# Kernel optimization log

Hardware: AMD Instinct MI355X
Metric: run time of the kernel (lower is better)

Reference implementation:

```python
import jax, jax.numpy as jnp
import numpy as np

EMBED_DIM = 4096
POLY_PTS = 32
POLY_DIM = POLY_PTS * 2  # 64
LN_EPS = 1e-5


def setup_inputs() -> dict:
    key = jax.random.key(0)
    ks = jax.random.split(key, 12)
    B, N, Dmax = 8, 1024, POLY_DIM
    s = 0.02
    return {
        "prompts": jax.random.normal(ks[0], (B, N, Dmax), dtype=jnp.float32),
        "prompt_types": jax.random.randint(ks[1], (B, N), 0, 3, dtype=jnp.int64),
        # point encoder: Linear(2, E)
        "point_w": jax.random.normal(ks[2], (EMBED_DIM, 2), dtype=jnp.float32) * s,
        "point_b": jax.random.normal(ks[3], (EMBED_DIM,), dtype=jnp.float32) * s,
        # box encoder: Linear(4, E)
        "box_w": jax.random.normal(ks[4], (EMBED_DIM, 4), dtype=jnp.float32) * s,
        "box_b": jax.random.normal(ks[5], (EMBED_DIM,), dtype=jnp.float32) * s,
        # polygon encoder: Linear(64,E) -> LayerNorm(E) -> ReLU -> Linear(E,E)
        "poly_w1": jax.random.normal(ks[6], (EMBED_DIM, POLY_DIM), dtype=jnp.float32) * s,
        "poly_b1": jax.random.normal(ks[7], (EMBED_DIM,), dtype=jnp.float32) * s,
        "ln_gamma": jnp.ones((EMBED_DIM,), dtype=jnp.float32),
        "ln_beta": jnp.zeros((EMBED_DIM,), dtype=jnp.float32),
        "poly_w2": jax.random.normal(ks[8], (EMBED_DIM, EMBED_DIM), dtype=jnp.float32) * s,
        "poly_b2": jax.random.normal(ks[9], (EMBED_DIM,), dtype=jnp.float32) * s,
        # type embedding table (3, E)
        "type_emb": jax.random.normal(ks[10], (3, EMBED_DIM), dtype=jnp.float32) * s,
    }


def _layernorm(x, gamma, beta):
    mu = jnp.mean(x, axis=-1, keepdims=True)
    var = jnp.mean(jnp.square(x - mu), axis=-1, keepdims=True)
    return (x - mu) * jax.lax.rsqrt(var + LN_EPS) * gamma + beta


def reference(prompts, prompt_types, point_w, point_b, box_w, box_b,
              poly_w1, poly_b1, ln_gamma, ln_beta, poly_w2, poly_b2, type_emb):
    # Per-type expert encodings computed densely, then selected by type mask
    # (same math as torch's masked gather -> linear -> scatter).
    pt = jnp.einsum('bnd,ed->bne', prompts[..., :2], point_w) + point_b + type_emb[0]
    bx = jnp.einsum('bnd,ed->bne', prompts[..., :4], box_w) + box_b + type_emb[1]
    h = jnp.einsum('bnd,ed->bne', prompts[..., :POLY_DIM], poly_w1) + poly_b1
    h = jax.nn.relu(_layernorm(h, ln_gamma, ln_beta))
    pg = jnp.einsum('bnd,ed->bne', h, poly_w2) + poly_b2 + type_emb[2]
    t = prompt_types[..., None]
    zeros = jnp.zeros_like(pt)
    out = jnp.where(t == 0, pt, zeros) + jnp.where(t == 1, bx, zeros) + jnp.where(t == 2, pg, zeros)
    return out
```

## Files before the change

kernel.cpp:

```cpp
#include <hip/hip_runtime.h>

#define EMBED 4096
#define NTOK 8192
#define LN_EPS 1e-5f

typedef float f4_t __attribute__((ext_vector_type(4)));
typedef __bf16 bf16x8 __attribute__((ext_vector_type(8)));
typedef unsigned short us8_t __attribute__((ext_vector_type(8)));

__device__ __forceinline__ unsigned short f2bf(float f) {
    unsigned int u = __float_as_uint(f);
    u += 0x7fffu + ((u >> 16) & 1u);
    return (unsigned short)(u >> 16);
}

typedef const __attribute__((address_space(1))) unsigned int gas_t;
typedef __attribute__((address_space(3))) unsigned int las_t;

__device__ __forceinline__ void gl_lds16(const void* g, void* l) {
    __builtin_amdgcn_global_load_lds((gas_t*)g, (las_t*)l, 16, 0, 0);
}

__global__ void k_compact(const int* __restrict__ types, int* __restrict__ idx,
                          int* __restrict__ counters) {
    __shared__ int cnt;
    if (threadIdx.x == 0) cnt = 0;
    __syncthreads();
    for (int i = threadIdx.x; i < NTOK; i += 1024) {
        if (types[i] == 2) {
            int s = atomicAdd(&cnt, 1);
            idx[s] = i;
        }
    }
    __syncthreads();
    if (threadIdx.x == 0) {
        counters[0] = cnt;
        counters[1] = (cnt + 127) & ~127;
    }
}

__global__ __launch_bounds__(256) void k_prepG(const float* __restrict__ w1,
                                               const float* __restrict__ b1,
                                               float* __restrict__ G,
                                               float* __restrict__ cbar) {
    int i = blockIdx.x;
    int t = threadIdx.x;
    float part[65];
#pragma unroll
    for (int j = 0; j < 65; ++j) part[j] = 0.f;
    for (int e = t; e < EMBED; e += 256) {
        const f4_t* row4 = (const f4_t*)(w1 + (size_t)e * 64);
        float be = b1[e];
        float ai = (i < 64) ? w1[(size_t)e * 64 + i] : ((i == 64) ? be : 1.f);
#pragma unroll
        for (int q = 0; q < 16; ++q) {
            f4_t r = row4[q];
            part[4 * q + 0] += ai * r.x;
            part[4 * q + 1] += ai * r.y;
            part[4 * q + 2] += ai * r.z;
            part[4 * q + 3] += ai * r.w;
        }
        part[64] += ai * be;
    }
#pragma unroll
    for (int j = 0; j < 65; ++j) {
        float v = part[j];
        v += __shfl_down(v, 32);
        v += __shfl_down(v, 16);
        v += __shfl_down(v, 8);
        v += __shfl_down(v, 4);
        v += __shfl_down(v, 2);
        v += __shfl_down(v, 1);
        part[j] = v;
    }
    __shared__ float sw[4][66];
    int wave = t >> 6, lane = t & 63;
    if (lane == 0) {
#pragma unroll
        for (int j = 0; j < 65; ++j) sw[wave][j] = part[j];
    }
    __syncthreads();
    if (t < 65) {
        float s = (sw[0][t] + sw[1][t] + sw[2][t] + sw[3][t]) * (1.f / 4096.f);
        if (i < 65) G[i * 65 + t] = s;
        else        cbar[t] = s;
    }
}

__global__ __launch_bounds__(256) void k_conv(const float* __restrict__ src,
                                              unsigned short* __restrict__ dst) {
    int i = blockIdx.x * 256 + threadIdx.x;
    const f4_t* in4 = (const f4_t*)src;
    f4_t v0 = in4[(size_t)i * 2];
    f4_t v1 = in4[(size_t)i * 2 + 1];
    us8_t o;
    o[0] = f2bf(v0.x); o[1] = f2bf(v0.y); o[2] = f2bf(v0.z); o[3] = f2bf(v0.w);
    o[4] = f2bf(v1.x); o[5] = f2bf(v1.y); o[6] = f2bf(v1.z); o[7] = f2bf(v1.w);
    *(us8_t*)(dst + (size_t)i * 8) = o;
}

__global__ __launch_bounds__(256) void k_enc01(const float* __restrict__ prompts,
                                               const int* __restrict__ types,
                                               const float* __restrict__ pw,
                                               const float* __restrict__ pb,
                                               const float* __restrict__ bw,
                                               const float* __restrict__ bb,
                                               const float* __restrict__ temb,
                                               float* __restrict__ out) {
    int token = blockIdx.x;
    int ty = types[token];
    if (ty >= 2) return;
    const float* x = prompts + (size_t)token * 64;
    float x0 = x[0], x1 = x[1], x2 = x[2], x3 = x[3];
    f4_t* o4 = (f4_t*)(out + (size_t)token * EMBED);
    int t = threadIdx.x;
    if (ty == 0) {
        const f4_t* w4 = (const f4_t*)pw;
        const f4_t* b4 = (const f4_t*)pb;
        const f4_t* te4 = (const f4_t*)temb;
#pragma unroll
        for (int j = 0; j < 4; ++j) {
            int e4 = t + 256 * j;
            f4_t wa = w4[e4 * 2], wb = w4[e4 * 2 + 1];
            f4_t bv = b4[e4], tv = te4[e4];
            f4_t r;
            r.x = x0 * wa.x + x1 * wa.y + bv.x + tv.x;
            r.y = x0 * wa.z + x1 * wa.w + bv.y + tv.y;
            r.z = x0 * wb.x + x1 * wb.y + bv.z + tv.z;
            r.w = x0 * wb.z + x1 * wb.w + bv.w + tv.w;
            o4[e4] = r;
        }
    } else {
        const f4_t* w4 = (const f4_t*)bw;
        const f4_t* b4 = (const f4_t*)bb;
        const f4_t* te4 = (const f4_t*)(temb + EMBED);
#pragma unroll
        for (int j = 0; j < 4; ++j) {
            int e4 = t + 256 * j;
            f4_t w0 = w4[e4 * 4 + 0], w1v = w4[e4 * 4 + 1];
            f4_t w2v = w4[e4 * 4 + 2], w3v = w4[e4 * 4 + 3];
            f4_t bv = b4[e4], tv = te4[e4];
            f4_t r;
            r.x = x0 * w0.x + x1 * w0.y + x2 * w0.z + x3 * w0.w + bv.x + tv.x;
            r.y = x0 * w1v.x + x1 * w1v.y + x2 * w1v.z + x3 * w1v.w + bv.y + tv.y;
            r.z = x0 * w2v.x + x1 * w2v.y + x2 * w2v.z + x3 * w2v.w + bv.z + tv.z;
            r.w = x0 * w3v.x + x1 * w3v.y + x2 * w3v.z + x3 * w3v.w + bv.w + tv.w;
            o4[e4] = r;
        }
    }
}

__global__ __launch_bounds__(256) void k_stats(const float* __restrict__ prompts,
                                               const int* __restrict__ idx,
                                               const int* __restrict__ counters,
                                               const float* __restrict__ cbar,
                                               const float* __restrict__ G,
                                               float* __restrict__ mu,
                                               float* __restrict__ rstd,
                                               unsigned short* __restrict__ xbuf) {
    int count = counters[0], padded = counters[1];
    int base = blockIdx.x * 4;
    if (base >= padded) return;
    __shared__ float sG[65 * 65];
    __shared__ __align__(16) float xs[4][66];
    int t = threadIdx.x;
    for (int v = t; v < 65 * 65; v += 256) sG[v] = G[v];
    int r = t >> 6, lane = t & 63;
    int m = base + r;
    bool vld = (m < count);
    float xv = vld ? prompts[(size_t)idx[m] * 64 + lane] : 0.f;
    xs[r][lane] = xv;
    if (lane == 0) xs[r][64] = vld ? 1.f : 0.f;
    xbuf[(size_t)m * 64 + lane] = vld ? f2bf(xv) : (unsigned short)0;
    __syncthreads();
    float mu_p, m2_p;
    {
        float xi = xs[r][lane];
        mu_p = cbar[lane] * xi;
        const float* Gr = sG + lane * 65;
        float rd = 0.f;
        for (int j = 0; j < 65; ++j) rd += Gr[j] * xs[r][j];
        m2_p = xi * rd;
    }
    if (lane == 0) {
        float xi = xs[r][64];
        mu_p += cbar[64] * xi;
        const float* Gr = sG + 64 * 65;
        float rd = 0.f;
        for (int j = 0; j < 65; ++j) rd += Gr[j] * xs[r][j];
        m2_p += xi * rd;
    }
    for (int off = 32; off > 0; off >>= 1) {
        mu_p += __shfl_down(mu_p, off);
        m2_p += __shfl_down(m2_p, off);
    }
    if (lane == 0) {
        if (vld) {
            mu[m] = mu_p;
            rstd[m] = rsqrtf(fmaxf(m2_p - mu_p * mu_p, 0.f) + LN_EPS);
        } else {
            mu[m] = 0.f;
            rstd[m] = 0.f;
        }
    }
}

__global__ __launch_bounds__(256) void k_lin1m(const unsigned short* __restrict__ xbuf,
                                               const unsigned short* __restrict__ w1b,
                                               const int* __restrict__ counters,
                                               const float* __restrict__ b1,
                                               const float* __restrict__ gamma,
                                               const float* __restrict__ beta,
                                               const float* __restrict__ mu,
                                               const float* __restrict__ rstd,
                                               unsigned short* __restrict__ hbuf) {
    int padded = counters[1];
    int m0 = blockIdx.y * 128;
    if (m0 >= padded) return;
    int n0 = blockIdx.x * 128;

    __shared__ unsigned short At[128 * 32];
    __shared__ unsigned short Bt[128 * 32];

    int t = threadIdx.x;
    int lane = t & 63, wave = t >> 6;
    int wm = (wave >> 1) * 64;
    int wn = (wave & 1) * 64;

    int srow = t >> 2, skg = t & 3;
    const unsigned short* Ag = xbuf + (size_t)(m0 + srow) * 64 + skg * 8;
    const unsigned short* Bg = w1b + (size_t)(n0 + srow) * 64 + skg * 8;
    char* AtC = (char*)At;
    char* BtC = (char*)Bt;
    int ldsw = (t & ~63) * 16;

    f4_t acc[4][4];
#pragma unroll
    for (int i = 0; i < 4; ++i)
#pragma unroll
        for (int j = 0; j < 4; ++j) acc[i][j] = (f4_t)0.f;

    int fr = lane & 15;
    int quad = lane >> 4;

#pragma unroll
    for (int k0 = 0; k0 < 64; k0 += 32) {
        __syncthreads();
        gl_lds16(Ag + k0,            AtC + ldsw);
        gl_lds16(Ag + 64 * 64 + k0,  AtC + 4096 + ldsw);
        gl_lds16(Bg + k0,            BtC + ldsw);
        gl_lds16(Bg + 64 * 64 + k0,  BtC + 4096 + ldsw);
        __syncthreads();

        bf16x8 a[4], b[4];
#pragma unroll
        for (int i = 0; i < 4; ++i) {
            a[i] = *(const bf16x8*)(AtC + (wm + i * 16 + fr) * 64 + quad * 16);
            b[i] = *(const bf16x8*)(BtC + (wn + i * 16 + fr) * 64 + quad * 16);
        }
#pragma unroll
        for (int i = 0; i < 4; ++i)
#pragma unroll
            for (int j = 0; j < 4; ++j)
                acc[i][j] = __builtin_amdgcn_mfma_f32_16x16x32_bf16(a[i], b[j], acc[i][j], 0, 0, 0);
    }

#pragma unroll
    for (int i = 0; i < 4; ++i) {
#pragma unroll
        for (int r = 0; r < 4; ++r) {
            int grow = m0 + wm + i * 16 + quad * 4 + r;
            float muv = mu[grow], rsv = rstd[grow];
            unsigned short* hrow = hbuf + (size_t)grow * EMBED;
#pragma unroll
            for (int j = 0; j < 4; ++j) {
                int gcol = n0 + wn + j * 16 + fr;
                float h = (acc[i][j][r] + b1[gcol] - muv) * rsv * gamma[gcol] + beta[gcol];
                hrow[gcol] = f2bf(fmaxf(h, 0.f));
            }
        }
    }
}

__global__ __launch_bounds__(256) void k_gemm(const unsigned short* __restrict__ hbuf,
                                              const unsigned short* __restrict__ w2b,
                                              const int* __restrict__ idx,
                                              const int* __restrict__ counters,
                                              const float* __restrict__ b2,
                                              const float* __restrict__ te2,
                                              float* __restrict__ out) {
    int count = counters[0], padded = counters[1];
    int m0 = blockIdx.y * 128;
    if (m0 >= padded) return;
    int n0 = blockIdx.x * 128;

    __shared__ unsigned short At[128 * 32];
    __shared__ unsigned short Bt[128 * 32];

    int t = threadIdx.x;
    int lane = t & 63, wave = t >> 6;
    int wm = (wave >> 1) * 64;
    int wn = (wave & 1) * 64;

    int srow = t >> 2, skg = t & 3;
    const unsigned short* Ag = hbuf + (size_t)(m0 + srow) * EMBED + skg * 8;
    const unsigned short* Bg = w2b + (size_t)(n0 + srow) * EMBED + skg * 8;
    char* AtC = (char*)At;
    char* BtC = (char*)Bt;
    int ldsw = (t & ~63) * 16;

    f4_t acc[4][4];
#pragma unroll
    for (int i = 0; i < 4; ++i)
#pragma unroll
        for (int j = 0; j < 4; ++j) acc[i][j] = (f4_t)0.f;

    int fr = lane & 15;
    int quad = lane >> 4;

    for (int k0 = 0; k0 < EMBED; k0 += 32) {
        __syncthreads();
        gl_lds16(Ag + k0,               AtC + ldsw);
        gl_lds16(Ag + 64 * EMBED + k0,  AtC + 4096 + ldsw);
        gl_lds16(Bg + k0,               BtC + ldsw);
        gl_lds16(Bg + 64 * EMBED + k0,  BtC + 4096 + ldsw);
        __syncthreads();

        bf16x8 a[4], b[4];
#pragma unroll
        for (int i = 0; i < 4; ++i) {
            a[i] = *(const bf16x8*)(AtC + (wm + i * 16 + fr) * 64 + quad * 16);
            b[i] = *(const bf16x8*)(BtC + (wn + i * 16 + fr) * 64 + quad * 16);
        }
#pragma unroll
        for (int i = 0; i < 4; ++i)
#pragma unroll
            for (int j = 0; j < 4; ++j)
                acc[i][j] = __builtin_amdgcn_mfma_f32_16x16x32_bf16(a[i], b[j], acc[i][j], 0, 0, 0);
    }

#pragma unroll
    for (int i = 0; i < 4; ++i) {
#pragma unroll
        for (int r = 0; r < 4; ++r) {
            int grow = m0 + wm + i * 16 + quad * 4 + r;
            if (grow < count) {
                float* orow = out + (size_t)idx[grow] * EMBED;
#pragma unroll
                for (int j = 0; j < 4; ++j) {
                    int gcol = n0 + wn + j * 16 + fr;
                    orow[gcol] = acc[i][j][r] + b2[gcol] + te2[gcol];
                }
            }
        }
    }
}

extern "C" void kernel_launch(void* const* d_in, const int* in_sizes, int n_in,
                              void* d_out, int out_size, void* d_ws, size_t ws_size,
                              hipStream_t stream) {
    const float* prompts  = (const float*)d_in[0];
    const int*   types    = (const int*)d_in[1];
    const float* point_w  = (const float*)d_in[2];
    const float* point_b  = (const float*)d_in[3];
    const float* box_w    = (const float*)d_in[4];
    const float* box_b    = (const float*)d_in[5];
    const float* poly_w1  = (const float*)d_in[6];
    const float* poly_b1  = (const float*)d_in[7];
    const float* ln_g     = (const float*)d_in[8];
    const float* ln_b     = (const float*)d_in[9];
    const float* poly_w2  = (const float*)d_in[10];
    const float* poly_b2  = (const float*)d_in[11];
    const float* type_emb = (const float*)d_in[12];
    float* out = (float*)d_out;

    char* ws = (char*)d_ws;
    int*   counters = (int*)ws;
    int*   idx      = (int*)(ws + 256);
    float* cbar     = (float*)(ws + 33280);
    float* G        = (float*)(ws + 33792);
    float* muarr    = (float*)(ws + 51200);
    float* rstdarr  = (float*)(ws + 84224);
    unsigned short* xbuf = (unsigned short*)(ws + 131072);
    unsigned short* w1b  = (unsigned short*)(ws + 131072 + 1048576);
    unsigned short* w2b  = (unsigned short*)(ws + 2097152);
    unsigned short* hbuf = (unsigned short*)(ws + 2097152 + (size_t)EMBED * EMBED * 2);

    k_compact<<<1, 1024, 0, stream>>>(types, idx, counters);
    k_prepG<<<66, 256, 0, stream>>>(poly_w1, poly_b1, G, cbar);
    k_conv<<<EMBED * EMBED / (256 * 8), 256, 0, stream>>>(poly_w2, w2b);
    k_conv<<<EMBED * 64 / (256 * 8), 256, 0, stream>>>(poly_w1, w1b);
    k_enc01<<<NTOK, 256, 0, stream>>>(prompts, types, point_w, point_b,
                                      box_w, box_b, type_emb, out);
    k_stats<<<NTOK / 4, 256, 0, stream>>>(prompts, idx, counters, cbar, G,
                                          muarr, rstdarr, xbuf);
    k_lin1m<<<dim3(EMBED / 128, NTOK / 128), 256, 0, stream>>>(
        xbuf, w1b, counters, poly_b1, ln_g, ln_b, muarr, rstdarr, hbuf);
    k_gemm<<<dim3(EMBED / 128, NTOK / 128), 256, 0, stream>>>(
        hbuf, w2b, idx, counters, poly_b2, type_emb + 2 * EMBED, out);
}
```

Measured before the change: 388.4 us.

## Fuse prep kernels into one launch and stage 64-wide K tiles in GEMMs

Merges the compaction, G/cbar precompute, both bf16 weight conversions and the point/box encoder into one block-indexed prep kernel. This removes four launches and lets the independent pieces run concurrently. The G precompute now splits its 65 output columns across waves, cutting per-thread register arrays from 65 to 17 entries. Both GEMMs now load two 32-wide K slices per barrier pair, halving the synchronisations in the main 4096-K loop, at the cost of double the LDS per block.

```diff
diff --git a/kernel.cpp b/kernel.cpp
--- a/kernel.cpp
+++ b/kernel.cpp
@@ -3,6 +3,9 @@
 #define EMBED 4096
 #define NTOK 8192
 #define LN_EPS 1e-5f
+
+#define NB_CONVW2 (EMBED * EMBED / (256 * 8))
+#define NB_CONVW1 (EMBED * 64 / (256 * 8))
 
 typedef float f4_t __attribute__((ext_vector_type(4)));
 typedef __bf16 bf16x8 __attribute__((ext_vector_type(8)));
@@ -21,75 +24,9 @@
     __builtin_amdgcn_global_load_lds((gas_t*)g, (las_t*)l, 16, 0, 0);
 }
 
-__global__ void k_compact(const int* __restrict__ types, int* __restrict__ idx,
-                          int* __restrict__ counters) {
-    __shared__ int cnt;
-    if (threadIdx.x == 0) cnt = 0;
-    __syncthreads();
-    for (int i = threadIdx.x; i < NTOK; i += 1024) {
-        if (types[i] == 2) {
-            int s = atomicAdd(&cnt, 1);
-            idx[s] = i;
-        }
-    }
-    __syncthreads();
-    if (threadIdx.x == 0) {
-        counters[0] = cnt;
-        counters[1] = (cnt + 127) & ~127;
-    }
-}
-
-__global__ __launch_bounds__(256) void k_prepG(const float* __restrict__ w1,
-                                               const float* __restrict__ b1,
-                                               float* __restrict__ G,
-                                               float* __restrict__ cbar) {
-    int i = blockIdx.x;
-    int t = threadIdx.x;
-    float part[65];
-#pragma unroll
-    for (int j = 0; j < 65; ++j) part[j] = 0.f;
-    for (int e = t; e < EMBED; e += 256) {
-        const f4_t* row4 = (const f4_t*)(w1 + (size_t)e * 64);
-        float be = b1[e];
-        float ai = (i < 64) ? w1[(size_t)e * 64 + i] : ((i == 64) ? be : 1.f);
-#pragma unroll
-        for (int q = 0; q < 16; ++q) {
-            f4_t r = row4[q];
-            part[4 * q + 0] += ai * r.x;
-            part[4 * q + 1] += ai * r.y;
-            part[4 * q + 2] += ai * r.z;
-            part[4 * q + 3] += ai * r.w;
-        }
-        part[64] += ai * be;
-    }
-#pragma unroll
-    for (int j = 0; j < 65; ++j) {
-        float v = part[j];
-        v += __shfl_down(v, 32);
-        v += __shfl_down(v, 16);
-        v += __shfl_down(v, 8);
-        v += __shfl_down(v, 4);
-        v += __shfl_down(v, 2);
-        v += __shfl_down(v, 1);
-        part[j] = v;
-    }
-    __shared__ float sw[4][66];
-    int wave = t >> 6, lane = t & 63;
-    if (lane == 0) {
-#pragma unroll
-        for (int j = 0; j < 65; ++j) sw[wave][j] = part[j];
-    }
-    __syncthreads();
-    if (t < 65) {
-        float s = (sw[0][t] + sw[1][t] + sw[2][t] + sw[3][t]) * (1.f / 4096.f);
-        if (i < 65) G[i * 65 + t] = s;
-        else        cbar[t] = s;
-    }
-}
-
-__global__ __launch_bounds__(256) void k_conv(const float* __restrict__ src,
-                                              unsigned short* __restrict__ dst) {
-    int i = blockIdx.x * 256 + threadIdx.x;
+__device__ __forceinline__ void conv_body(const float* __restrict__ src,
+                                          unsigned short* __restrict__ dst,
+                                          int i) {
     const f4_t* in4 = (const f4_t*)src;
     f4_t v0 = in4[(size_t)i * 2];
     f4_t v1 = in4[(size_t)i * 2 + 1];
@@ -99,53 +36,136 @@
     *(us8_t*)(dst + (size_t)i * 8) = o;
 }
 
-__global__ __launch_bounds__(256) void k_enc01(const float* __restrict__ prompts,
-                                               const int* __restrict__ types,
-                                               const float* __restrict__ pw,
-                                               const float* __restrict__ pb,
-                                               const float* __restrict__ bw,
-                                               const float* __restrict__ bb,
-                                               const float* __restrict__ temb,
-                                               float* __restrict__ out) {
-    int token = blockIdx.x;
-    int ty = types[token];
-    if (ty >= 2) return;
-    const float* x = prompts + (size_t)token * 64;
-    float x0 = x[0], x1 = x[1], x2 = x[2], x3 = x[3];
-    f4_t* o4 = (f4_t*)(out + (size_t)token * EMBED);
+__global__ __launch_bounds__(256) void k_prep(
+    const float* __restrict__ prompts, const int* __restrict__ types,
+    const float* __restrict__ pw, const float* __restrict__ pb,
+    const float* __restrict__ bw, const float* __restrict__ bb,
+    const float* __restrict__ temb,
+    const float* __restrict__ w1, const float* __restrict__ b1,
+    const float* __restrict__ w2,
+    int* __restrict__ idx, int* __restrict__ counters,
+    float* __restrict__ G, float* __restrict__ cbar,
+    unsigned short* __restrict__ w1b, unsigned short* __restrict__ w2b,
+    float* __restrict__ out)
+{
+    int bid = blockIdx.x;
     int t = threadIdx.x;
-    if (ty == 0) {
-        const f4_t* w4 = (const f4_t*)pw;
-        const f4_t* b4 = (const f4_t*)pb;
-        const f4_t* te4 = (const f4_t*)temb;
-#pragma unroll
-        for (int j = 0; j < 4; ++j) {
-            int e4 = t + 256 * j;
-            f4_t wa = w4[e4 * 2], wb = w4[e4 * 2 + 1];
-            f4_t bv = b4[e4], tv = te4[e4];
-            f4_t r;
-            r.x = x0 * wa.x + x1 * wa.y + bv.x + tv.x;
-            r.y = x0 * wa.z + x1 * wa.w + bv.y + tv.y;
-            r.z = x0 * wb.x + x1 * wb.y + bv.z + tv.z;
-            r.w = x0 * wb.z + x1 * wb.w + bv.w + tv.w;
-            o4[e4] = r;
-        }
-    } else {
-        const f4_t* w4 = (const f4_t*)bw;
-        const f4_t* b4 = (const f4_t*)bb;
-        const f4_t* te4 = (const f4_t*)(temb + EMBED);
-#pragma unroll
-        for (int j = 0; j < 4; ++j) {
-            int e4 = t + 256 * j;
-            f4_t w0 = w4[e4 * 4 + 0], w1v = w4[e4 * 4 + 1];
-            f4_t w2v = w4[e4 * 4 + 2], w3v = w4[e4 * 4 + 3];
-            f4_t bv = b4[e4], tv = te4[e4];
-            f4_t r;
-            r.x = x0 * w0.x + x1 * w0.y + x2 * w0.z + x3 * w0.w + bv.x + tv.x;
-            r.y = x0 * w1v.x + x1 * w1v.y + x2 * w1v.z + x3 * w1v.w + bv.y + tv.y;
-            r.z = x0 * w2v.x + x1 * w2v.y + x2 * w2v.z + x3 * w2v.w + bv.z + tv.z;
-            r.w = x0 * w3v.x + x1 * w3v.y + x2 * w3v.z + x3 * w3v.w + bv.w + tv.w;
-            o4[e4] = r;
+
+    if (bid == 0) {
+        __shared__ int cnt;
+        if (t == 0) cnt = 0;
+        __syncthreads();
+        for (int i = t; i < NTOK; i += 256) {
+            if (types[i] == 2) {
+                int s = atomicAdd(&cnt, 1);
+                idx[s] = i;
+            }
+        }
+        __syncthreads();
+        if (t == 0) {
+            counters[0] = cnt;
+            counters[1] = (cnt + 127) & ~127;
+        }
+        return;
+    }
+
+    if (bid <= 66) {
+        int i = bid - 1;
+        int wave = t >> 6, lane = t & 63;
+        float part[17];
+#pragma unroll
+        for (int jj = 0; jj < 17; ++jj) part[jj] = 0.f;
+        for (int e = lane; e < EMBED; e += 64) {
+            const f4_t* row4 = (const f4_t*)(w1 + (size_t)e * 64);
+            float be = b1[e];
+            float ai = (i < 64) ? w1[(size_t)e * 64 + i] : ((i == 64) ? be : 1.f);
+            f4_t r0 = row4[wave * 4 + 0];
+            f4_t r1 = row4[wave * 4 + 1];
+            f4_t r2 = row4[wave * 4 + 2];
+            f4_t r3 = row4[wave * 4 + 3];
+            part[0]  += ai * r0.x; part[1]  += ai * r0.y;
+            part[2]  += ai * r0.z; part[3]  += ai * r0.w;
+            part[4]  += ai * r1.x; part[5]  += ai * r1.y;
+            part[6]  += ai * r1.z; part[7]  += ai * r1.w;
+            part[8]  += ai * r2.x; part[9]  += ai * r2.y;
+            part[10] += ai * r2.z; part[11] += ai * r2.w;
+            part[12] += ai * r3.x; part[13] += ai * r3.y;
+            part[14] += ai * r3.z; part[15] += ai * r3.w;
+            if (wave == 3) part[16] += ai * be;
+        }
+#pragma unroll
+        for (int jj = 0; jj < 17; ++jj) {
+            float v = part[jj];
+            v += __shfl_down(v, 32);
+            v += __shfl_down(v, 16);
+            v += __shfl_down(v, 8);
+            v += __shfl_down(v, 4);
+            v += __shfl_down(v, 2);
+            v += __shfl_down(v, 1);
+            part[jj] = v;
+        }
+        if (lane == 0) {
+            int nj = (wave == 3) ? 17 : 16;
+            for (int jj = 0; jj < nj; ++jj) {
+                int j = (jj == 16) ? 64 : (wave * 16 + jj);
+                float s = part[jj] * (1.f / 4096.f);
+                if (i < 65) G[i * 65 + j] = s;
+                else        cbar[j] = s;
+            }
+        }
+        return;
+    }
+
+    if (bid < 67 + NB_CONVW2) {
+        conv_body(w2, w2b, (bid - 67) * 256 + t);
+        return;
+    }
+
+    if (bid < 67 + NB_CONVW2 + NB_CONVW1) {
+        conv_body(w1, w1b, (bid - 67 - NB_CONVW2) * 256 + t);
+        return;
+    }
+
+    {
+        int token = bid - (67 + NB_CONVW2 + NB_CONVW1);
+        int ty = types[token];
+        if (ty >= 2) return;
+        const float* x = prompts + (size_t)token * 64;
+        float x0 = x[0], x1 = x[1], x2 = x[2], x3 = x[3];
+        f4_t* o4 = (f4_t*)(out + (size_t)token * EMBED);
+        if (ty == 0) {
+            const f4_t* w4 = (const f4_t*)pw;
+            const f4_t* b4 = (const f4_t*)pb;
+            const f4_t* te4 = (const f4_t*)temb;
+#pragma unroll
+            for (int j = 0; j < 4; ++j) {
+                int e4 = t + 256 * j;
+                f4_t wa = w4[e4 * 2], wb = w4[e4 * 2 + 1];
+                f4_t bv = b4[e4], tv = te4[e4];
+                f4_t r;
+                r.x = x0 * wa.x + x1 * wa.y + bv.x + tv.x;
+                r.y = x0 * wa.z + x1 * wa.w + bv.y + tv.y;
+                r.z = x0 * wb.x + x1 * wb.y + bv.z + tv.z;
+                r.w = x0 * wb.z + x1 * wb.w + bv.w + tv.w;
+                o4[e4] = r;
+            }
+        } else {
+            const f4_t* w4 = (const f4_t*)bw;
+            const f4_t* b4 = (const f4_t*)bb;
+            const f4_t* te4 = (const f4_t*)(temb + EMBED);
+#pragma unroll
+            for (int j = 0; j < 4; ++j) {
+                int e4 = t + 256 * j;
+                f4_t w0 = w4[e4 * 4 + 0], w1v = w4[e4 * 4 + 1];
+                f4_t w2v = w4[e4 * 4 + 2], w3v = w4[e4 * 4 + 3];
+                f4_t bv = b4[e4], tv = te4[e4];
+                f4_t r;
+                r.x = x0 * w0.x + x1 * w0.y + x2 * w0.z + x3 * w0.w + bv.x + tv.x;
+                r.y = x0 * w1v.x + x1 * w1v.y + x2 * w1v.z + x3 * w1v.w + bv.y + tv.y;
+                r.z = x0 * w2v.x + x1 * w2v.y + x2 * w2v.z + x3 * w2v.w + bv.z + tv.z;
+                r.w = x0 * w3v.x + x1 * w3v.y + x2 * w3v.z + x3 * w3v.w + bv.w + tv.w;
+                o4[e4] = r;
+            }
         }
     }
 }
@@ -219,8 +239,8 @@
     if (m0 >= padded) return;
     int n0 = blockIdx.x * 128;
 
-    __shared__ unsigned short At[128 * 32];
-    __shared__ unsigned short Bt[128 * 32];
+    __shared__ unsigned short At[2][128 * 32];
+    __shared__ unsigned short Bt[2][128 * 32];
 
     int t = threadIdx.x;
     int lane = t & 63, wave = t >> 6;
@@ -230,8 +250,8 @@
     int srow = t >> 2, skg = t & 3;
     const unsigned short* Ag = xbuf + (size_t)(m0 + srow) * 64 + skg * 8;
     const unsigned short* Bg = w1b + (size_t)(n0 + srow) * 64 + skg * 8;
-    char* AtC = (char*)At;
-    char* BtC = (char*)Bt;
+    char* A0 = (char*)At[0]; char* A1 = (char*)At[1];
+    char* B0 = (char*)Bt[0]; char* B1 = (char*)Bt[1];
     int ldsw = (t & ~63) * 16;
 
     f4_t acc[4][4];
@@ -243,20 +263,32 @@
     int fr = lane & 15;
     int quad = lane >> 4;
 
-#pragma unroll
-    for (int k0 = 0; k0 < 64; k0 += 32) {
-        __syncthreads();
-        gl_lds16(Ag + k0,            AtC + ldsw);
-        gl_lds16(Ag + 64 * 64 + k0,  AtC + 4096 + ldsw);
-        gl_lds16(Bg + k0,            BtC + ldsw);
-        gl_lds16(Bg + 64 * 64 + k0,  BtC + 4096 + ldsw);
-        __syncthreads();
-
+    gl_lds16(Ag,                A0 + ldsw);
+    gl_lds16(Ag + 64 * 64,      A0 + 4096 + ldsw);
+    gl_lds16(Ag + 32,           A1 + ldsw);
+    gl_lds16(Ag + 64 * 64 + 32, A1 + 4096 + ldsw);
+    gl_lds16(Bg,                B0 + ldsw);
+    gl_lds16(Bg + 64 * 64,      B0 + 4096 + ldsw);
+    gl_lds16(Bg + 32,           B1 + ldsw);
+    gl_lds16(Bg + 64 * 64 + 32, B1 + 4096 + ldsw);
+    __syncthreads();
+
+    {
         bf16x8 a[4], b[4];
 #pragma unroll
         for (int i = 0; i < 4; ++i) {
-            a[i] = *(const bf16x8*)(AtC + (wm + i * 16 + fr) * 64 + quad * 16);
-            b[i] = *(const bf16x8*)(BtC + (wn + i * 16 + fr) * 64 + quad * 16);
+            a[i] = *(const bf16x8*)(A0 + (wm + i * 16 + fr) * 64 + quad * 16);
+            b[i] = *(const bf16x8*)(B0 + (wn + i * 16 + fr) * 64 + quad * 16);
+        }
+#pragma unroll
+        for (int i = 0; i < 4; ++i)
+#pragma unroll
+            for (int j = 0; j < 4; ++j)
+                acc[i][j] = __builtin_amdgcn_mfma_f32_16x16x32_bf16(a[i], b[j], acc[i][j], 0, 0, 0);
+#pragma unroll
+        for (int i = 0; i < 4; ++i) {
+            a[i] = *(const bf16x8*)(A1 + (wm + i * 16 + fr) * 64 + quad * 16);
+            b[i] = *(const bf16x8*)(B1 + (wn + i * 16 + fr) * 64 + quad * 16);
         }
 #pragma unroll
         for (int i = 0; i < 4; ++i)
@@ -294,8 +326,8 @@
     if (m0 >= padded) return;
     int n0 = blockIdx.x * 128;
 
-    __shared__ unsigned short At[128 * 32];
-    __shared__ unsigned short Bt[128 * 32];
+    __shared__ unsigned short At[2][128 * 32];
+    __shared__ unsigned short Bt[2][128 * 32];
 
     int t = threadIdx.x;
     int lane = t & 63, wave = t >> 6;
@@ -305,8 +337,8 @@
     int srow = t >> 2, skg = t & 3;
     const unsigned short* Ag = hbuf + (size_t)(m0 + srow) * EMBED + skg * 8;
     const unsigned short* Bg = w2b + (size_t)(n0 + srow) * EMBED + skg * 8;
-    char* AtC = (char*)At;
-    char* BtC = (char*)Bt;
+    char* A0 = (char*)At[0]; char* A1 = (char*)At[1];
+    char* B0 = (char*)Bt[0]; char* B1 = (char*)Bt[1];
     int ldsw = (t & ~63) * 16;
 
     f4_t acc[4][4];
@@ -318,19 +350,33 @@
     int fr = lane & 15;
     int quad = lane >> 4;
 
-    for (int k0 = 0; k0 < EMBED; k0 += 32) {
+    for (int k0 = 0; k0 < EMBED; k0 += 64) {
         __syncthreads();
-        gl_lds16(Ag + k0,               AtC + ldsw);
-        gl_lds16(Ag + 64 * EMBED + k0,  AtC + 4096 + ldsw);
-        gl_lds16(Bg + k0,               BtC + ldsw);
-        gl_lds16(Bg + 64 * EMBED + k0,  BtC + 4096 + ldsw);
+        gl_lds16(Ag + k0,                   A0 + ldsw);
+        gl_lds16(Ag + 64 * EMBED + k0,      A0 + 4096 + ldsw);
+        gl_lds16(Ag + k0 + 32,              A1 + ldsw);
+        gl_lds16(Ag + 64 * EMBED + k0 + 32, A1 + 4096 + ldsw);
+        gl_lds16(Bg + k0,                   B0 + ldsw);
+        gl_lds16(Bg + 64 * EMBED + k0,      B0 + 4096 + ldsw);
+        gl_lds16(Bg + k0 + 32,              B1 + ldsw);
+        gl_lds16(Bg + 64 * EMBED + k0 + 32, B1 + 4096 + ldsw);
         __syncthreads();
 
         bf16x8 a[4], b[4];
 #pragma unroll
         for (int i = 0; i < 4; ++i) {
-            a[i] = *(const bf16x8*)(AtC + (wm + i * 16 + fr) * 64 + quad * 16);
-            b[i] = *(const bf16x8*)(BtC + (wn + i * 16 + fr) * 64 + quad * 16);
+            a[i] = *(const bf16x8*)(A0 + (wm + i * 16 + fr) * 64 + quad * 16);
+            b[i] = *(const bf16x8*)(B0 + (wn + i * 16 + fr) * 64 + quad * 16);
+        }
+#pragma unroll
+        for (int i = 0; i < 4; ++i)
+#pragma unroll
+            for (int j = 0; j < 4; ++j)
+                acc[i][j] = __builtin_amdgcn_mfma_f32_16x16x32_bf16(a[i], b[j], acc[i][j], 0, 0, 0);
+#pragma unroll
+        for (int i = 0; i < 4; ++i) {
+            a[i] = *(const bf16x8*)(A1 + (wm + i * 16 + fr) * 64 + quad * 16);
+            b[i] = *(const bf16x8*)(B1 + (wn + i * 16 + fr) * 64 + quad * 16);
         }
 #pragma unroll
         for (int i = 0; i < 4; ++i)
@@ -386,12 +432,11 @@
     unsigned short* w2b  = (unsigned short*)(ws + 2097152);
     unsigned short* hbuf = (unsigned short*)(ws + 2097152 + (size_t)EMBED * EMBED * 2);
 
-    k_compact<<<1, 1024, 0, stream>>>(types, idx, counters);
-    k_prepG<<<66, 256, 0, stream>>>(poly_w1, poly_b1, G, cbar);
-    k_conv<<<EMBED * EMBED / (256 * 8), 256, 0, stream>>>(poly_w2, w2b);
-    k_conv<<<EMBED * 64 / (256 * 8), 256, 0, stream>>>(poly_w1, w1b);
-    k_enc01<<<NTOK, 256, 0, stream>>>(prompts, types, point_w, point_b,
-                                      box_w, box_b, type_emb, out);
+    int nprep = 67 + NB_CONVW2 + NB_CONVW1 + NTOK;
+    k_prep<<<nprep, 256, 0, stream>>>(prompts, types, point_w, point_b,
+                                      box_w, box_b, type_emb,
+                                      poly_w1, poly_b1, poly_w2,
+                                      idx, counters, G, cbar, w1b, w2b, out);
     k_stats<<<NTOK / 4, 256, 0, stream>>>(prompts, idx, counters, cbar, G,
                                           muarr, rstdarr, xbuf);
     k_lin1m<<<dim3(EMBED / 128, NTOK / 128), 256, 0, stream>>>(
```

Result: slower. 404.5 us (+4.1%).
